# Performance work log

Hardware: AMD Instinct MI355X
Metric: run time of the kernel (lower is better)

Reference implementation:

```python
import math
import jax, jax.numpy as jnp
import numpy as np

B, L = 2, 4096
D_MODEL, D_STATE, D_CONV, EXPAND = 1024, 64, 4, 2
D_INNER = EXPAND * D_MODEL
DT_RANK = max(1, D_MODEL // 16)
EPS = float(jnp.finfo(jnp.float32).eps)  # torch nn.RMSNorm default eps


def setup_inputs() -> dict:
    key = jax.random.key(0)
    ks = jax.random.split(key, 8)
    sc = lambda k, shape, scale: jax.random.normal(k, shape, jnp.float32) * scale
    x = jax.random.normal(ks[0], (B, L, D_MODEL), jnp.float32)
    in_proj_w = sc(ks[1], (2 * D_INNER, D_MODEL), D_MODEL ** -0.5)
    conv_w = sc(ks[2], (D_INNER, 1, D_CONV), D_CONV ** -0.5)  # depthwise kernel
    conv_b = jnp.zeros((D_INNER,), jnp.float32)
    norm_w = jnp.ones((D_INNER,), jnp.float32)
    dt_std = DT_RANK ** -0.5
    dt_w = jax.random.uniform(ks[3], (D_INNER, D_INNER), jnp.float32, -dt_std, dt_std)
    dt_b = jnp.full((D_INNER,), math.log(0.5), jnp.float32)
    A_log = jnp.log(jnp.tile(jnp.arange(1, D_STATE + 1, dtype=jnp.float32), (D_INNER, 1)))
    D = jnp.ones((D_INNER,), jnp.float32)
    B_w = sc(ks[4], (D_STATE, D_INNER), D_INNER ** -0.5)
    C_w = sc(ks[5], (D_STATE, D_INNER), D_INNER ** -0.5)
    out_w = sc(ks[6], (D_MODEL, D_INNER), D_INNER ** -0.5)
    return dict(x=x, in_proj_w=in_proj_w, conv_w=conv_w, conv_b=conv_b,
                norm_w=norm_w, dt_w=dt_w, dt_b=dt_b, A_log=A_log, D=D,
                B_w=B_w, C_w=C_w, out_w=out_w)


def _mamba2_fwd(x, in_proj_w, conv_w, conv_b, norm_w, dt_w, dt_b, A_log, D, B_w, C_w, out_w):
    batch, seq_len, _ = x.shape
    # input projection + gating
    xg = x @ in_proj_w.T                               # [B, L, 2*d_inner]
    x_inner, gate = jnp.split(xg, 2, axis=-1)
    x_inner = x_inner * jax.nn.silu(gate)
    # causal depthwise conv1d (left pad d_conv-1, keep first L outputs)
    lhs = x_inner.transpose(0, 2, 1)                   # [B, d_inner, L]
    conv = jax.lax.conv_general_dilated(
        lhs, conv_w, window_strides=(1,), padding=[(D_CONV - 1, 0)],
        feature_group_count=conv_w.shape[0])
    x_conv = (conv + conv_b[None, :, None]).transpose(0, 2, 1)  # [B, L, d_inner]
    # RMSNorm
    x_conv = x_conv * jax.lax.rsqrt(jnp.mean(x_conv ** 2, axis=-1, keepdims=True) + EPS) * norm_w
    # SSM parameters
    dt = jax.nn.softplus(x_conv @ dt_w.T + dt_b)       # [B, L, d_inner]
    A = -jnp.exp(A_log)                                # [d_inner, d_state]
    Bt = x_conv @ B_w.T                                # [B, L, d_state]
    Ct = x_conv @ C_w.T                                # [B, L, d_state]

    # selective scan: h_t = exp(dt_t * A) * h_{t-1} + dt_t * B_t * x_t
    def step(h, inp):
        dt_t, b_t, c_t, xc_t = inp                     # [B,d], [B,N], [B,N], [B,d]
        A_bar = jnp.exp(dt_t[..., None] * A)           # [B, d_inner, d_state]
        h = A_bar * h + (dt_t * xc_t)[..., None] * b_t[:, None, :]
        y_t = jnp.einsum('bdn,bn->bd', h, c_t)
        return h, y_t

    h0 = jnp.zeros((batch, x_conv.shape[-1], D_STATE), x_conv.dtype)
    xs = (dt.transpose(1, 0, 2), Bt.transpose(1, 0, 2),
          Ct.transpose(1, 0, 2), x_conv.transpose(1, 0, 2))
    _, ys = jax.lax.scan(step, h0, xs)                 # ys: [L, B, d_inner]
    y = ys.transpose(1, 0, 2) + D * x_conv             # skip connection
    return y @ out_w.T                                 # [B, L, d_model]


def reference(x, in_proj_w, conv_w, conv_b, norm_w, dt_w, dt_b, A_log, D, B_w, C_w, out_w):
    return _mamba2_fwd(x, in_proj_w, conv_w, conv_b, norm_w, dt_w, dt_b, A_log, D, B_w, C_w, out_w)
```

## Files before the change

kernel.cpp:

```cpp
#include <hip/hip_runtime.h>
#include <cmath>

#define BB 2
#define LL 4096
#define DM 1024
#define DI 2048
#define NS 64
static constexpr float EPSF  = 1.1920928955078125e-07f;
static constexpr float LOG2E = 1.4426950408889634f;

typedef unsigned short u16;
typedef __attribute__((ext_vector_type(4))) unsigned short u16x4;
typedef __attribute__((ext_vector_type(8))) short bf16x8;
typedef __attribute__((ext_vector_type(4))) float f32x4;

__device__ __forceinline__ u16 f2bf(float f){
    unsigned u = __float_as_uint(f);
    return (u16)((u + 0x7fffu + ((u >> 16) & 1u)) >> 16);
}
__device__ __forceinline__ float bf2f(u16 h){ return __uint_as_float(((unsigned)h) << 16); }
__device__ __forceinline__ void gload16(const void* g, void* l){
    __builtin_amdgcn_global_load_lds((const __attribute__((address_space(1))) void*)g,
                                     (__attribute__((address_space(3))) void*)l, 16, 0, 0);
}

__global__ __launch_bounds__(256)
void cvt_all(const float* __restrict__ s0, const float* __restrict__ s1,
             const float* __restrict__ s2, const float* __restrict__ s3,
             const float* __restrict__ s4, const float* __restrict__ s5,
             u16* __restrict__ d0, u16* __restrict__ d1, u16* __restrict__ d2,
             u16* __restrict__ d3, u16* __restrict__ d4, u16* __restrict__ d5)
{
    size_t v = (size_t)blockIdx.x * 256 + threadIdx.x;
    const float* src; u16* dst; size_t off;
    if      (v < 2097152u){ src=s0; dst=d0; off=v; }
    else if (v < 3145728u){ src=s1; dst=d1; off=v-2097152u; }
    else if (v < 4194304u){ src=s2; dst=d2; off=v-3145728u; }
    else if (v < 4227072u){ src=s3; dst=d3; off=v-4194304u; }
    else if (v < 4259840u){ src=s4; dst=d4; off=v-4227072u; }
    else                  { src=s5; dst=d5; off=v-4259840u; }
    size_t i = off*4;
    float4 x = *(const float4*)(src+i);
    u16x4 o; o[0]=f2bf(x.x); o[1]=f2bf(x.y); o[2]=f2bf(x.z); o[3]=f2bf(x.w);
    *(u16x4*)(dst+i) = o;
}

template<int MODE, int OUTBF>
__global__ __launch_bounds__(256)
void gemm_bf16(const u16* __restrict__ A, const u16* __restrict__ W,
               const float* __restrict__ bias, void* __restrict__ Cout,
               int M, int N, int K)
{
    __shared__ u16 As[128*32];
    __shared__ u16 Bs[128*32];
    __shared__ u16 Bg[(MODE==1) ? 128*32 : 8];

    const int tid  = threadIdx.x;
    const int lane = tid & 63;
    const int wave = tid >> 6;
    const int m0 = blockIdx.y * 128;
    const int n0 = blockIdx.x * 128;
    const int wr = wave >> 1, wc = wave & 1;

    f32x4 acc [4][4];
    f32x4 acc2[(MODE==1)?4:1][(MODE==1)?4:1];
    #pragma unroll
    for (int i=0;i<4;i++)
        #pragma unroll
        for (int j=0;j<4;j++)
            #pragma unroll
            for (int r=0;r<4;r++) acc[i][j][r] = 0.f;
    if (MODE==1){
        #pragma unroll
        for (int i=0;i<4;i++)
            #pragma unroll
            for (int j=0;j<4;j++)
                #pragma unroll
                for (int r=0;r<4;r++) acc2[i][j][r] = 0.f;
    }

    for (int k0 = 0; k0 < K; k0 += 32) {
        #pragma unroll
        for (int it = 0; it < 2; ++it) {
            const int s  = it*256 + tid;
            const int r  = s >> 2;
            const int q  = s & 3;
            const int qs = q ^ ((r >> 1) & 3);
            const int ub = (it*256 + wave*64) * 8;
            gload16(A + (size_t)(m0 + r)*K + k0 + qs*8, As + ub);
            gload16(W + (size_t)(n0 + r)*K + k0 + qs*8, Bs + ub);
            if (MODE==1)
                gload16(W + (size_t)(N + n0 + r)*K + k0 + qs*8, Bg + ub);
        }
        __syncthreads();

        bf16x8 af[4], bfr[4], bgr[(MODE==1)?4:1];
        #pragma unroll
        for (int mi=0; mi<4; ++mi){
            const int r  = wr*64 + mi*16 + (lane & 15);
            const int qs = (lane >> 4) ^ ((r >> 1) & 3);
            af[mi] = *(const bf16x8*)(As + (r*4 + qs)*8);
        }
        #pragma unroll
        for (int ni=0; ni<4; ++ni){
            const int c  = wc*64 + ni*16 + (lane & 15);
            const int qs = (lane >> 4) ^ ((c >> 1) & 3);
            bfr[ni] = *(const bf16x8*)(Bs + (c*4 + qs)*8);
            if (MODE==1) bgr[ni] = *(const bf16x8*)(Bg + (c*4 + qs)*8);
        }
        #pragma unroll
        for (int mi=0; mi<4; ++mi)
            #pragma unroll
            for (int ni=0; ni<4; ++ni){
                acc[mi][ni] = __builtin_amdgcn_mfma_f32_16x16x32_bf16(af[mi], bfr[ni], acc[mi][ni], 0,0,0);
                if (MODE==1)
                    acc2[mi][ni] = __builtin_amdgcn_mfma_f32_16x16x32_bf16(af[mi], bgr[ni], acc2[mi][ni], 0,0,0);
            }
        __syncthreads();
    }

    #pragma unroll
    for (int mi=0; mi<4; ++mi){
        #pragma unroll
        for (int ni=0; ni<4; ++ni){
            const int col = n0 + wc*64 + ni*16 + (lane & 15);
            if (MODE==5 && n0 < 2048){
                u16x4 o;
                #pragma unroll
                for (int rj=0; rj<4; ++rj){
                    float z = acc[mi][ni][rj] + bias[col];
                    float v = (z > 20.f) ? z : log1pf(__expf(z));
                    o[rj] = f2bf(v);
                }
                const int rb = m0 + wr*64 + mi*16 + (lane >> 4)*4;
                const int bb = rb >> 12;
                const int l  = rb & (LL-1);
                *(u16x4*)((u16*)Cout + ((size_t)bb*DI + col)*LL + l) = o;
            } else if (MODE==5){
                const int n2 = col - 2048;
                float* bcd = (float*)((u16*)Cout + (size_t)2*BB*DI*LL);
                #pragma unroll
                for (int rj=0; rj<4; ++rj){
                    const int row = m0 + wr*64 + mi*16 + (lane >> 4)*4 + rj;
                    bcd[((size_t)row*64 + (n2 & 63))*2 + (n2 >> 6)] = acc[mi][ni][rj];
                }
            } else {
                #pragma unroll
                for (int rj=0; rj<4; ++rj){
                    const int row = m0 + wr*64 + mi*16 + (lane >> 4)*4 + rj;
                    float v = acc[mi][ni][rj];
                    if (MODE==1){
                        float g = acc2[mi][ni][rj];
                        v = v * (g / (1.f + __expf(-g)));
                    }
                    if (OUTBF) ((u16*)Cout)[(size_t)row*N + col] = f2bf(v);
                    else       ((float*)Cout)[(size_t)row*N + col] = v;
                }
            }
        }
    }
}

__global__ __launch_bounds__(256)
void conv_rms(const u16* __restrict__ xin, const float* __restrict__ cw,
              const float* __restrict__ cb, const float* __restrict__ nw,
              u16* __restrict__ xc)
{
    const int bl  = blockIdx.x;
    const int l   = bl & (LL-1);
    const int tid = threadIdx.x;
    const int d0  = tid * 8;

    float a[8];
    #pragma unroll
    for (int j=0;j<8;j++) a[j] = cb[d0+j];
    #pragma unroll
    for (int t=0;t<4;t++){
        const int ls = l - 3 + t;
        if (ls >= 0){
            bf16x8 xv = *(const bf16x8*)(xin + (size_t)(bl-3+t)*DI + d0);
            #pragma unroll
            for (int j=0;j<8;j++)
                a[j] += bf2f((u16)xv[j]) * cw[(d0+j)*4 + t];
        }
    }
    float ss = 0.f;
    #pragma unroll
    for (int j=0;j<8;j++) ss += a[j]*a[j];
    ss += __shfl_xor(ss,32); ss += __shfl_xor(ss,16); ss += __shfl_xor(ss,8);
    ss += __shfl_xor(ss,4);  ss += __shfl_xor(ss,2);  ss += __shfl_xor(ss,1);
    __shared__ float red[4];
    if ((tid & 63)==0) red[tid>>6] = ss;
    __syncthreads();
    const float tot   = red[0]+red[1]+red[2]+red[3];
    const float scale = rsqrtf(tot * (1.f/DI) + EPSF);
    u16x4 o0, o1;
    #pragma unroll
    for (int j=0;j<4;j++) o0[j] = f2bf(a[j]  *scale*nw[d0+j]);
    #pragma unroll
    for (int j=0;j<4;j++) o1[j] = f2bf(a[4+j]*scale*nw[d0+4+j]);
    *(u16x4*)(xc + (size_t)bl*DI + d0)     = o0;
    *(u16x4*)(xc + (size_t)bl*DI + d0 + 4) = o1;
}

__global__ __launch_bounds__(256)
void transpose_bf(const u16* __restrict__ in, u16* __restrict__ out, int R, int C)
{
    __shared__ u16 t[32][36];
    const int b  = blockIdx.z;
    const int r0 = blockIdx.y * 32;
    const int c0 = blockIdx.x * 32;
    const int ir = threadIdx.x >> 3;
    const int ic = (threadIdx.x & 7) * 4;
    const size_t base = (size_t)b * R * C;

    u16x4 v = *(const u16x4*)(in + base + (size_t)(r0+ir)*C + c0 + ic);
    #pragma unroll
    for (int k=0;k<4;k++) t[ir][ic+k] = v[k];
    __syncthreads();
    u16x4 o;
    #pragma unroll
    for (int k=0;k<4;k++) o[k] = t[ic+k][ir];
    *(u16x4*)(out + base + (size_t)(c0+ir)*R + r0 + ic) = o;
}

#define BSTAGE(MU) \
    { _Pragma("unroll") \
      for (int i=0;i<MU;i++){ \
          const bool g = (lane & MU) != 0; \
          float q = g ? p[i] : p[i+MU]; \
          float r = __shfl_xor(q, MU); \
          p[i] = (g ? p[i+MU] : p[i]) + r; \
      } }

__global__ __launch_bounds__(512)
void scan9(const u16* __restrict__ dtT, const u16* __restrict__ xcT,
           const float* __restrict__ BCi, const float* __restrict__ A_log,
           const float* __restrict__ Dp, u16* __restrict__ yT)
{
    __shared__ float lbc[2][64*128];
    __shared__ float dtu[8][64][2];
    const int tid  = threadIdx.x;
    const int lane = tid & 63;
    const int wave = tid >> 6;
    const int b    = blockIdx.x >> 8;
    const int d    = (blockIdx.x & 255) * 8 + wave;

    const float Ac = -__expf(A_log[d*NS + lane]) * LOG2E;
    const float Dd = Dp[d];
    const size_t chbase = ((size_t)b*DI + d) * LL;
    const u16* dtp = dtT + chbase;
    const u16* xcp = xcT + chbase;
    u16*       yp  = yT  + chbase;
    const float* bcb = BCi + (size_t)b * LL * 128;

    auto stage = [&](int t0, int bufi){
        const float* src = bcb + (size_t)t0 * 128;
        #pragma unroll
        for (int i=0;i<4;i++){
            const int slot = i*512 + wave*64;
            gload16(src + (size_t)(slot + lane)*4, &lbc[bufi][slot*4]);
        }
    };

    stage(0, 0);
    asm volatile("s_waitcnt vmcnt(0)" ::: "memory");
    __syncthreads();

    float h = 0.f;
    int cur = 0;
    for (int t0 = 0; t0 < LL; t0 += 64) {
        if (t0 + 64 < LL) stage(t0 + 64, cur ^ 1);

        const float dtL = bf2f(dtp[t0 + lane]);
        const float xcL = bf2f(xcp[t0 + lane]);
        *(float2*)&dtu[wave][lane][0] = make_float2(dtL, dtL * xcL);
        const float* lb = lbc[cur];
        const float* dub = &dtu[wave][0][0];

        float p[64];
        #pragma unroll
        for (int j=0;j<64;j++){
            const float2 du = *(const float2*)(dub + j*2);
            const float2 bc = *(const float2*)(lb + (j*64 + lane)*2);
            const float a   = exp2f(du.x * Ac);
            h = a*h + du.y*bc.x;
            p[j] = h * bc.y;
        }
        #pragma unroll
        for (int i=0;i<32;i++){
            float a0 = p[i], b0 = p[i+32];
            asm("v_permlane32_swap_b32 %0, %1" : "+v"(a0), "+v"(b0));
            p[i] = a0 + b0;
        }
        BSTAGE(16) BSTAGE(8) BSTAGE(4) BSTAGE(2) BSTAGE(1)
        {
            float yv = p[0] + Dd * xcL;
            unsigned pk;
            asm("v_cvt_pk_bf16_f32 %0, %1, %2" : "=v"(pk) : "v"(yv), "v"(yv));
            yp[t0 + lane] = (u16)pk;
        }

        asm volatile("s_waitcnt vmcnt(0)" ::: "memory");
        __syncthreads();
        cur ^= 1;
    }
}

extern "C" void kernel_launch(void* const* d_in, const int* in_sizes, int n_in,
                              void* d_out, int out_size, void* d_ws, size_t ws_size,
                              hipStream_t stream) {
    const float* x       = (const float*)d_in[0];
    const float* in_proj = (const float*)d_in[1];
    const float* conv_w  = (const float*)d_in[2];
    const float* conv_b  = (const float*)d_in[3];
    const float* norm_w  = (const float*)d_in[4];
    const float* dt_w    = (const float*)d_in[5];
    const float* dt_b    = (const float*)d_in[6];
    const float* A_log   = (const float*)d_in[7];
    const float* Dp      = (const float*)d_in[8];
    const float* B_w     = (const float*)d_in[9];
    const float* C_w     = (const float*)d_in[10];
    const float* out_w   = (const float*)d_in[11];

    const int M = BB * LL;
    u16* wsu = (u16*)d_ws;
    u16*   x_bf   = wsu;
    u16*   ip_bf  = wsu + (size_t)M*DM;
    u16*   dtw_bf = ip_bf + (size_t)2*DI*DM;
    u16*   bcw_bf = dtw_bf + (size_t)DI*DI;
    u16*   xin_bf = bcw_bf + (size_t)128*DI;
    u16*   xc_bf  = xin_bf + (size_t)M*DI;
    float* BC     = (float*)(xc_bf + (size_t)M*DI);
    u16*   ow_bf  = (u16*)(BC + (size_t)M*128);
    u16*   dtT_bf = xin_bf;
    u16*   xcT_bf = x_bf;
    u16*   yT_bf  = xc_bf;
    u16*   y_bf   = xin_bf;

    cvt_all<<<18688, 256, 0, stream>>>(x, in_proj, dt_w, B_w, C_w, out_w,
                                       x_bf, ip_bf, dtw_bf, bcw_bf,
                                       bcw_bf + (size_t)NS*DI, ow_bf);

    gemm_bf16<1,1><<<dim3(DI/128, M/128), 256, 0, stream>>>(
        x_bf, ip_bf, nullptr, xin_bf, M, DI, DM);

    conv_rms<<<M, 256, 0, stream>>>(xin_bf, conv_w, conv_b, norm_w, xc_bf);

    gemm_bf16<5,1><<<dim3(2176/128, M/128), 256, 0, stream>>>(
        xc_bf, dtw_bf, dt_b, dtT_bf, M, 2176, DI);

    transpose_bf<<<dim3(DI/32, LL/32, BB), 256, 0, stream>>>(xc_bf, xcT_bf, LL, DI);

    scan9<<<BB*DI/8, 512, 0, stream>>>(dtT_bf, xcT_bf, BC, A_log, Dp, yT_bf);

    transpose_bf<<<dim3(LL/32, DI/32, BB), 256, 0, stream>>>(yT_bf, y_bf, DI, LL);

    gemm_bf16<0,0><<<dim3(DM/128, M/128), 256, 0, stream>>>(
        y_bf, ow_bf, nullptr, (float*)d_out, M, DM, DI);
}
```

Measured before the change: 964.2 us.

## Process two channels per wave in scan kernel to reuse staged B/C loads

Each wave in the selective-scan kernel now handles two d_inner channels instead of one, so every B/C value read from LDS feeds two independent recurrences. The grid shrinks from 512 to 256 blocks. This halves LDS B/C traffic and the number of BC staging passes per channel, and gives two independent dependency chains per iteration for more instruction-level parallelism. The cost is doubled register pressure (two 64-element partial arrays) and only 256 blocks, which may leave compute units underfilled or force spills.

Result: slower. 1.019 ms (+5.7%).

```diff
diff --git a/kernel.cpp b/kernel.cpp
--- a/kernel.cpp
+++ b/kernel.cpp
@@ -224,34 +224,38 @@
     *(u16x4*)(out + base + (size_t)(c0+ir)*R + r0 + ic) = o;
 }
 
-#define BSTAGE(MU) \
+#define BSTG(P, MU) \
     { _Pragma("unroll") \
       for (int i=0;i<MU;i++){ \
           const bool g = (lane & MU) != 0; \
-          float q = g ? p[i] : p[i+MU]; \
+          float q = g ? P[i] : P[i+MU]; \
           float r = __shfl_xor(q, MU); \
-          p[i] = (g ? p[i+MU] : p[i]) + r; \
+          P[i] = (g ? P[i+MU] : P[i]) + r; \
       } }
 
 __global__ __launch_bounds__(512)
-void scan9(const u16* __restrict__ dtT, const u16* __restrict__ xcT,
-           const float* __restrict__ BCi, const float* __restrict__ A_log,
-           const float* __restrict__ Dp, u16* __restrict__ yT)
+void scan11(const u16* __restrict__ dtT, const u16* __restrict__ xcT,
+            const float* __restrict__ BCi, const float* __restrict__ A_log,
+            const float* __restrict__ Dp, u16* __restrict__ yT)
 {
     __shared__ float lbc[2][64*128];
-    __shared__ float dtu[8][64][2];
+    __shared__ float dtu[8][64][4];
     const int tid  = threadIdx.x;
     const int lane = tid & 63;
     const int wave = tid >> 6;
-    const int b    = blockIdx.x >> 8;
-    const int d    = (blockIdx.x & 255) * 8 + wave;
-
-    const float Ac = -__expf(A_log[d*NS + lane]) * LOG2E;
-    const float Dd = Dp[d];
-    const size_t chbase = ((size_t)b*DI + d) * LL;
-    const u16* dtp = dtT + chbase;
-    const u16* xcp = xcT + chbase;
-    u16*       yp  = yT  + chbase;
+    const int b    = blockIdx.x >> 7;
+    const int d0   = (blockIdx.x & 127) * 16 + wave * 2;
+    const int d1   = d0 + 1;
+
+    const float Ac0 = -__expf(A_log[d0*NS + lane]) * LOG2E;
+    const float Ac1 = -__expf(A_log[d1*NS + lane]) * LOG2E;
+    const float Dd0 = Dp[d0];
+    const float Dd1 = Dp[d1];
+    const size_t ch0 = ((size_t)b*DI + d0) * LL;
+    const size_t ch1 = ((size_t)b*DI + d1) * LL;
+    const u16* dtp0 = dtT + ch0;  const u16* dtp1 = dtT + ch1;
+    const u16* xcp0 = xcT + ch0;  const u16* xcp1 = xcT + ch1;
+    u16* yp0 = yT + ch0;          u16* yp1 = yT + ch1;
     const float* bcb = BCi + (size_t)b * LL * 128;
 
     auto stage = [&](int t0, int bufi){
@@ -267,38 +271,51 @@
     asm volatile("s_waitcnt vmcnt(0)" ::: "memory");
     __syncthreads();
 
-    float h = 0.f;
+    float h0 = 0.f, h1 = 0.f;
     int cur = 0;
     for (int t0 = 0; t0 < LL; t0 += 64) {
         if (t0 + 64 < LL) stage(t0 + 64, cur ^ 1);
 
-        const float dtL = bf2f(dtp[t0 + lane]);
-        const float xcL = bf2f(xcp[t0 + lane]);
-        *(float2*)&dtu[wave][lane][0] = make_float2(dtL, dtL * xcL);
+        const float dtL0 = bf2f(dtp0[t0 + lane]);
+        const float xcL0 = bf2f(xcp0[t0 + lane]);
+        const float dtL1 = bf2f(dtp1[t0 + lane]);
+        const float xcL1 = bf2f(xcp1[t0 + lane]);
+        *(float4*)&dtu[wave][lane][0] =
+            make_float4(dtL0, dtL0 * xcL0, dtL1, dtL1 * xcL1);
         const float* lb = lbc[cur];
         const float* dub = &dtu[wave][0][0];
 
-        float p[64];
+        float p0[64], p1[64];
         #pragma unroll
         for (int j=0;j<64;j++){
-            const float2 du = *(const float2*)(dub + j*2);
+            const float4 du = *(const float4*)(dub + j*4);
             const float2 bc = *(const float2*)(lb + (j*64 + lane)*2);
-            const float a   = exp2f(du.x * Ac);
-            h = a*h + du.y*bc.x;
-            p[j] = h * bc.y;
+            const float a0  = exp2f(du.x * Ac0);
+            const float a1  = exp2f(du.z * Ac1);
+            h0 = a0*h0 + du.y*bc.x;
+            h1 = a1*h1 + du.w*bc.x;
+            p0[j] = h0 * bc.y;
+            p1[j] = h1 * bc.y;
         }
         #pragma unroll
         for (int i=0;i<32;i++){
-            float a0 = p[i], b0 = p[i+32];
+            float a0 = p0[i], b0 = p0[i+32];
             asm("v_permlane32_swap_b32 %0, %1" : "+v"(a0), "+v"(b0));
-            p[i] = a0 + b0;
-        }
-        BSTAGE(16) BSTAGE(8) BSTAGE(4) BSTAGE(2) BSTAGE(1)
+            p0[i] = a0 + b0;
+            float a1v = p1[i], b1v = p1[i+32];
+            asm("v_permlane32_swap_b32 %0, %1" : "+v"(a1v), "+v"(b1v));
+            p1[i] = a1v + b1v;
+        }
+        BSTG(p0,16) BSTG(p0,8) BSTG(p0,4) BSTG(p0,2) BSTG(p0,1)
+        BSTG(p1,16) BSTG(p1,8) BSTG(p1,4) BSTG(p1,2) BSTG(p1,1)
         {
-            float yv = p[0] + Dd * xcL;
-            unsigned pk;
-            asm("v_cvt_pk_bf16_f32 %0, %1, %2" : "=v"(pk) : "v"(yv), "v"(yv));
-            yp[t0 + lane] = (u16)pk;
+            float yv0 = p0[0] + Dd0 * xcL0;
+            float yv1 = p1[0] + Dd1 * xcL1;
+            unsigned pk0, pk1;
+            asm("v_cvt_pk_bf16_f32 %0, %1, %2" : "=v"(pk0) : "v"(yv0), "v"(yv0));
+            asm("v_cvt_pk_bf16_f32 %0, %1, %2" : "=v"(pk1) : "v"(yv1), "v"(yv1));
+            yp0[t0 + lane] = (u16)pk0;
+            yp1[t0 + lane] = (u16)pk1;
         }
 
         asm volatile("s_waitcnt vmcnt(0)" ::: "memory");
@@ -352,7 +369,7 @@
 
     transpose_bf<<<dim3(DI/32, LL/32, BB), 256, 0, stream>>>(xc_bf, xcT_bf, LL, DI);
 
-    scan9<<<BB*DI/8, 512, 0, stream>>>(dtT_bf, xcT_bf, BC, A_log, Dp, yT_bf);
+    scan11<<<256, 512, 0, stream>>>(dtT_bf, xcT_bf, BC, A_log, Dp, yT_bf);
 
     transpose_bf<<<dim3(LL/32, DI/32, BB), 256, 0, stream>>>(yT_bf, y_bf, DI, LL);
 
```

## Add 256x256 double-buffered GEMM for in_proj and dt projections, split B/C GEMM

Applied to the files above, without the earlier changes.

Adds a new 512-thread GEMM kernel with 256x256 tiles, K=64 double-buffered LDS staging, staged waitcnt/barrier interleaving and setprio around MFMA blocks. It is used for the gated input projection and the dt projection. For the input projection, the weight rows are interleaved during bf16 conversion so that x and gate columns land in the same tile, which lets one accumulator set compute the SiLU gating. The B/C projection is moved out of the dt GEMM into its own small 128-tile GEMM launch. The intent is higher MFMA utilisation and more operand reuse on the large GEMMs, at the cost of high register and LDS use (128 KB LDS per block) and lower occupancy.

After: 936.3 us. 1.03x faster.

```diff
diff --git a/kernel.cpp b/kernel.cpp
--- a/kernel.cpp
+++ b/kernel.cpp
@@ -33,27 +33,172 @@
 {
     size_t v = (size_t)blockIdx.x * 256 + threadIdx.x;
     const float* src; u16* dst; size_t off;
-    if      (v < 2097152u){ src=s0; dst=d0; off=v; }
-    else if (v < 3145728u){ src=s1; dst=d1; off=v-2097152u; }
-    else if (v < 4194304u){ src=s2; dst=d2; off=v-3145728u; }
-    else if (v < 4227072u){ src=s3; dst=d3; off=v-4194304u; }
-    else if (v < 4259840u){ src=s4; dst=d4; off=v-4227072u; }
-    else                  { src=s5; dst=d5; off=v-4259840u; }
+    int seg;
+    if      (v < 2097152u){ src=s0; dst=d0; off=v; seg=0; }
+    else if (v < 3145728u){ src=s1; dst=d1; off=v-2097152u; seg=1; }
+    else if (v < 4194304u){ src=s2; dst=d2; off=v-3145728u; seg=2; }
+    else if (v < 4227072u){ src=s3; dst=d3; off=v-4194304u; seg=3; }
+    else if (v < 4259840u){ src=s4; dst=d4; off=v-4227072u; seg=4; }
+    else                  { src=s5; dst=d5; off=v-4259840u; seg=5; }
     size_t i = off*4;
-    float4 x = *(const float4*)(src+i);
+    size_t isrc = i;
+    if (seg == 1){
+        size_t r = i >> 10, c = i & 1023;
+        size_t g = r >> 6, w6 = r & 63;
+        size_t s = (w6 < 32) ? (g*32 + w6) : (2048 + g*32 + (w6 - 32));
+        isrc = s*1024 + c;
+    }
+    float4 x = *(const float4*)(src+isrc);
     u16x4 o; o[0]=f2bf(x.x); o[1]=f2bf(x.y); o[2]=f2bf(x.z); o[3]=f2bf(x.w);
     *(u16x4*)(dst+i) = o;
 }
 
-template<int MODE, int OUTBF>
+template<int EPI>
+__global__ __launch_bounds__(512)
+void gemm256(const u16* __restrict__ A, const u16* __restrict__ W,
+             const float* __restrict__ bias, u16* __restrict__ out,
+             int M, int N, int K)
+{
+    __shared__ u16 Adb[2][256*64];
+    __shared__ u16 Bdb[2][256*64];
+    const int tid  = threadIdx.x;
+    const int lane = tid & 63;
+    const int w    = tid >> 6;
+    const int n0 = blockIdx.x * 256;
+    const int m0 = blockIdx.y * 256;
+    const int NT = K >> 6;
+
+    f32x4 acc[2][16];
+    #pragma unroll
+    for (int mf=0; mf<2; mf++)
+        #pragma unroll
+        for (int nf=0; nf<16; nf++)
+            #pragma unroll
+            for (int r=0;r<4;r++) acc[mf][nf][r] = 0.f;
+
+    auto stageA = [&](int kt, int buf){
+        const int k0 = kt << 6;
+        #pragma unroll
+        for (int i=0;i<4;i++){
+            const int s = i*512 + tid;
+            const int row = s >> 3;
+            const int q = (s & 7) ^ (row & 7);
+            gload16(A + (size_t)(m0+row)*K + k0 + q*8, &Adb[buf][s*8]);
+        }
+    };
+    auto stageBh = [&](int kt, int nh, int buf){
+        const int k0 = kt << 6;
+        #pragma unroll
+        for (int i=0;i<2;i++){
+            const int s = i*512 + tid;
+            const int row = nh*128 + (s >> 3);
+            const int q = (s & 7) ^ (row & 7);
+            gload16(W + (size_t)(n0+row)*K + k0 + q*8, &Bdb[buf][nh*8192 + s*8]);
+        }
+    };
+
+    bf16x8 af[2][2];
+    bf16x8 bfr[8];
+    auto readA = [&](int ks, int buf){
+        #pragma unroll
+        for (int mf=0; mf<2; mf++){
+            const int row = w*32 + mf*16 + (lane & 15);
+            const int q = (ks*4 + (lane >> 4)) ^ (row & 7);
+            af[ks][mf] = *(const bf16x8*)(&Adb[buf][row*64 + q*8]);
+        }
+    };
+    auto readB = [&](int nh, int ks, int buf){
+        #pragma unroll
+        for (int nf=0; nf<8; nf++){
+            const int row = nh*128 + nf*16 + (lane & 15);
+            const int q = (ks*4 + (lane >> 4)) ^ (row & 7);
+            bfr[nf] = *(const bf16x8*)(&Bdb[buf][row*64 + q*8]);
+        }
+    };
+    auto mfma16 = [&](int nbase, int ks){
+        __builtin_amdgcn_s_setprio(1);
+        #pragma unroll
+        for (int nf=0; nf<8; nf++)
+            #pragma unroll
+            for (int mf=0; mf<2; mf++)
+                acc[mf][nbase+nf] = __builtin_amdgcn_mfma_f32_16x16x32_bf16(
+                    af[ks][mf], bfr[nf], acc[mf][nbase+nf], 0,0,0);
+        __builtin_amdgcn_s_setprio(0);
+    };
+
+    stageA(0, 0); stageBh(0, 0, 0); stageBh(0, 1, 0);
+
+    int cur = 0;
+    for (int kt = 0; kt < NT; ++kt){
+        const int nb = cur ^ 1;
+        const bool pre = (kt + 1 < NT);
+        if (pre) asm volatile("s_waitcnt vmcnt(2)" ::: "memory");
+        else     asm volatile("s_waitcnt vmcnt(0)" ::: "memory");
+        __builtin_amdgcn_s_barrier();
+        if (pre) stageA(kt+1, nb);
+        readA(0, cur); readB(0, 0, cur);
+        mfma16(0, 0);
+        if (pre) asm volatile("s_waitcnt vmcnt(4)" ::: "memory");
+        __builtin_amdgcn_s_barrier();
+        if (pre) stageBh(kt+1, 0, nb);
+        readB(1, 0, cur);
+        mfma16(8, 0);
+        __builtin_amdgcn_s_barrier();
+        if (pre) stageBh(kt+1, 1, nb);
+        readA(1, cur); readB(0, 1, cur);
+        mfma16(0, 1);
+        __builtin_amdgcn_s_barrier();
+        readB(1, 1, cur);
+        mfma16(8, 1);
+        cur = nb;
+    }
+
+    if (EPI == 0){
+        #pragma unroll
+        for (int mf=0; mf<2; mf++)
+            #pragma unroll
+            for (int g4=0; g4<4; g4++)
+                #pragma unroll
+                for (int nf2=0; nf2<2; nf2++){
+                    const int na = g4*4 + nf2;
+                    const int d  = (n0 >> 1) + g4*32 + nf2*16 + (lane & 15);
+                    #pragma unroll
+                    for (int rj=0; rj<4; rj++){
+                        const int m = m0 + w*32 + mf*16 + (lane >> 4)*4 + rj;
+                        float v = acc[mf][na][rj];
+                        float g = acc[mf][na+2][rj];
+                        v = v * (g / (1.f + __expf(-g)));
+                        out[(size_t)m*DI + d] = f2bf(v);
+                    }
+                }
+    } else {
+        #pragma unroll
+        for (int mf=0; mf<2; mf++)
+            #pragma unroll
+            for (int na=0; na<16; na++){
+                const int col = n0 + na*16 + (lane & 15);
+                u16x4 o;
+                #pragma unroll
+                for (int rj=0; rj<4; rj++){
+                    float z = acc[mf][na][rj] + bias[col];
+                    float v = (z > 20.f) ? z : log1pf(__expf(z));
+                    o[rj] = f2bf(v);
+                }
+                const int rb = m0 + w*32 + mf*16 + (lane >> 4)*4;
+                const int bb = rb >> 12;
+                const int l  = rb & (LL-1);
+                *(u16x4*)(out + ((size_t)bb*DI + col)*LL + l) = o;
+            }
+    }
+}
+
+template<int MODE>
 __global__ __launch_bounds__(256)
 void gemm_bf16(const u16* __restrict__ A, const u16* __restrict__ W,
-               const float* __restrict__ bias, void* __restrict__ Cout,
-               int M, int N, int K)
+               void* __restrict__ Cout, int M, int N, int K)
 {
     __shared__ u16 As[128*32];
     __shared__ u16 Bs[128*32];
-    __shared__ u16 Bg[(MODE==1) ? 128*32 : 8];
 
     const int tid  = threadIdx.x;
     const int lane = tid & 63;
@@ -62,22 +207,13 @@
     const int n0 = blockIdx.x * 128;
     const int wr = wave >> 1, wc = wave & 1;
 
-    f32x4 acc [4][4];
-    f32x4 acc2[(MODE==1)?4:1][(MODE==1)?4:1];
+    f32x4 acc[4][4];
     #pragma unroll
     for (int i=0;i<4;i++)
         #pragma unroll
         for (int j=0;j<4;j++)
             #pragma unroll
             for (int r=0;r<4;r++) acc[i][j][r] = 0.f;
-    if (MODE==1){
-        #pragma unroll
-        for (int i=0;i<4;i++)
-            #pragma unroll
-            for (int j=0;j<4;j++)
-                #pragma unroll
-                for (int r=0;r<4;r++) acc2[i][j][r] = 0.f;
-    }
 
     for (int k0 = 0; k0 < K; k0 += 32) {
         #pragma unroll
@@ -89,12 +225,10 @@
             const int ub = (it*256 + wave*64) * 8;
             gload16(A + (size_t)(m0 + r)*K + k0 + qs*8, As + ub);
             gload16(W + (size_t)(n0 + r)*K + k0 + qs*8, Bs + ub);
-            if (MODE==1)
-                gload16(W + (size_t)(N + n0 + r)*K + k0 + qs*8, Bg + ub);
         }
         __syncthreads();
 
-        bf16x8 af[4], bfr[4], bgr[(MODE==1)?4:1];
+        bf16x8 af[4], bfr[4];
         #pragma unroll
         for (int mi=0; mi<4; ++mi){
             const int r  = wr*64 + mi*16 + (lane & 15);
@@ -106,16 +240,12 @@
             const int c  = wc*64 + ni*16 + (lane & 15);
             const int qs = (lane >> 4) ^ ((c >> 1) & 3);
             bfr[ni] = *(const bf16x8*)(Bs + (c*4 + qs)*8);
-            if (MODE==1) bgr[ni] = *(const bf16x8*)(Bg + (c*4 + qs)*8);
         }
         #pragma unroll
         for (int mi=0; mi<4; ++mi)
             #pragma unroll
-            for (int ni=0; ni<4; ++ni){
+            for (int ni=0; ni<4; ++ni)
                 acc[mi][ni] = __builtin_amdgcn_mfma_f32_16x16x32_bf16(af[mi], bfr[ni], acc[mi][ni], 0,0,0);
-                if (MODE==1)
-                    acc2[mi][ni] = __builtin_amdgcn_mfma_f32_16x16x32_bf16(af[mi], bgr[ni], acc2[mi][ni], 0,0,0);
-            }
         __syncthreads();
     }
 
@@ -124,38 +254,14 @@
         #pragma unroll
         for (int ni=0; ni<4; ++ni){
             const int col = n0 + wc*64 + ni*16 + (lane & 15);
-            if (MODE==5 && n0 < 2048){
-                u16x4 o;
-                #pragma unroll
-                for (int rj=0; rj<4; ++rj){
-                    float z = acc[mi][ni][rj] + bias[col];
-                    float v = (z > 20.f) ? z : log1pf(__expf(z));
-                    o[rj] = f2bf(v);
-                }
-                const int rb = m0 + wr*64 + mi*16 + (lane >> 4)*4;
-                const int bb = rb >> 12;
-                const int l  = rb & (LL-1);
-                *(u16x4*)((u16*)Cout + ((size_t)bb*DI + col)*LL + l) = o;
-            } else if (MODE==5){
-                const int n2 = col - 2048;
-                float* bcd = (float*)((u16*)Cout + (size_t)2*BB*DI*LL);
-                #pragma unroll
-                for (int rj=0; rj<4; ++rj){
-                    const int row = m0 + wr*64 + mi*16 + (lane >> 4)*4 + rj;
-                    bcd[((size_t)row*64 + (n2 & 63))*2 + (n2 >> 6)] = acc[mi][ni][rj];
-                }
-            } else {
-                #pragma unroll
-                for (int rj=0; rj<4; ++rj){
-                    const int row = m0 + wr*64 + mi*16 + (lane >> 4)*4 + rj;
-                    float v = acc[mi][ni][rj];
-                    if (MODE==1){
-                        float g = acc2[mi][ni][rj];
-                        v = v * (g / (1.f + __expf(-g)));
-                    }
-                    if (OUTBF) ((u16*)Cout)[(size_t)row*N + col] = f2bf(v);
-                    else       ((float*)Cout)[(size_t)row*N + col] = v;
-                }
+            #pragma unroll
+            for (int rj=0; rj<4; ++rj){
+                const int row = m0 + wr*64 + mi*16 + (lane >> 4)*4 + rj;
+                float v = acc[mi][ni][rj];
+                if (MODE==3)
+                    ((float*)Cout)[((size_t)row*64 + (col & 63))*2 + (col >> 6)] = v;
+                else
+                    ((float*)Cout)[(size_t)row*N + col] = v;
             }
         }
     }
@@ -342,13 +448,16 @@
                                        x_bf, ip_bf, dtw_bf, bcw_bf,
                                        bcw_bf + (size_t)NS*DI, ow_bf);
 
-    gemm_bf16<1,1><<<dim3(DI/128, M/128), 256, 0, stream>>>(
-        x_bf, ip_bf, nullptr, xin_bf, M, DI, DM);
+    gemm256<0><<<dim3(2*DI/256, M/256), 512, 0, stream>>>(
+        x_bf, ip_bf, nullptr, xin_bf, M, 2*DI, DM);
 
     conv_rms<<<M, 256, 0, stream>>>(xin_bf, conv_w, conv_b, norm_w, xc_bf);
 
-    gemm_bf16<5,1><<<dim3(2176/128, M/128), 256, 0, stream>>>(
-        xc_bf, dtw_bf, dt_b, dtT_bf, M, 2176, DI);
+    gemm256<1><<<dim3(DI/256, M/256), 512, 0, stream>>>(
+        xc_bf, dtw_bf, dt_b, dtT_bf, M, DI, DI);
+
+    gemm_bf16<3><<<dim3(1, M/128), 256, 0, stream>>>(
+        xc_bf, bcw_bf, BC, M, 128, DI);
 
     transpose_bf<<<dim3(DI/32, LL/32, BB), 256, 0, stream>>>(xc_bf, xcT_bf, LL, DI);
 
@@ -356,6 +465,6 @@
 
     transpose_bf<<<dim3(LL/32, DI/32, BB), 256, 0, stream>>>(yT_bf, y_bf, DI, LL);
 
-    gemm_bf16<0,0><<<dim3(DM/128, M/128), 256, 0, stream>>>(
-        y_bf, ow_bf, nullptr, (float*)d_out, M, DM, DI);
-}
+    gemm_bf16<0><<<dim3(DM/128, M/128), 256, 0, stream>>>(
+        y_bf, ow_bf, (float*)d_out, M, DM, DI);
+}
```
